# Kernel optimization log

Measured on AMD Instinct MI355X. Metric: run time of the kernel, lower is better.

## Reference

```python
import jax, jax.numpy as jnp
import numpy as np

HIDDEN = 1024
HEADS = 16
SCALE_EXP = 0.2  # module: scale = hidden_size ** (-scale)


def setup_inputs() -> dict:
    key = jax.random.key(0)
    k1, k2, k3, k4, k5 = jax.random.split(key, 5)
    b, s, h = 2, 2048, HIDDEN
    std = 1.0 / np.sqrt(h)
    return {
        "sequence_embedding": jax.random.normal(k1, (b, s, h), dtype=jnp.float32),
        "kqv_w": jax.random.normal(k2, (h, 3 * h), dtype=jnp.float32) * std,
        "kqv_b": jax.random.normal(k3, (3 * h,), dtype=jnp.float32) * std,
        "ff_w": jax.random.normal(k4, (h, h), dtype=jnp.float32) * std,
        "ff_b": jax.random.normal(k5, (h,), dtype=jnp.float32) * std,
    }


def reference(sequence_embedding, kqv_w, kqv_b, ff_w, ff_b):
    b, s, hid = sequence_embedding.shape
    d = hid // HEADS
    scale = hid ** (-SCALE_EXP)
    kqv = sequence_embedding @ kqv_w + kqv_b  # [b, s, 3h]
    k, q, v = jnp.split(kqv, 3, axis=-1)
    split_heads = lambda x: x.reshape(b, s, HEADS, d).transpose(0, 2, 1, 3)  # b h s d
    k, q, v = split_heads(k), split_heads(q), split_heads(v)
    # scores[s, n] = k_s . q_n  (rows = key pos, cols = query pos)
    scores = jnp.einsum('bhsd,bhnd->bhsn', k, q) * scale
    # faithful to source: softmax over last axis n (the QUERY axis)
    attn = jax.nn.softmax(scores, axis=-1)
    # sum over s (key positions); output indexed by n
    out = jnp.einsum('bhsn,bhsd->bhnd', attn, v)  # [b, h, s, d]
    out = out.transpose(0, 2, 1, 3).reshape(b, s, hid)
    return out @ ff_w + ff_b  # dropout is identity at inference
```

## Files before the change

kernel.cpp:

```cpp
#include <hip/hip_runtime.h>

typedef unsigned short u16;
typedef unsigned int   u32;
typedef __attribute__((ext_vector_type(8))) short s16x8;
typedef __attribute__((ext_vector_type(4))) float f32x4;

#define B_   2
#define S_   2048
#define HID  1024
#define NH   16
#define N3   3072
#define M_   4096
#define C2   0.36067376022224085f
#define OFF2 12.0f

__device__ __forceinline__ u16 f2b(float f) {
  union { float f; u32 u; } v; v.f = f;
  u32 r = (v.u + 0x7FFFu + ((v.u >> 16) & 1u)) >> 16;
  return (u16)r;
}

__device__ __forceinline__ u32 cvt_pk_bf16(float lo, float hi) {
  u32 r;
  asm("v_cvt_pk_bf16_f32 %0, %1, %2" : "=v"(r) : "v"(lo), "v"(hi));
  return r;
}

#define GLL(gp, lp)                                                          \
  __builtin_amdgcn_global_load_lds(                                          \
      (const __attribute__((address_space(1))) void*)(gp),                   \
      (__attribute__((address_space(3))) void*)(lp), 16, 0, 0)

__global__ __launch_bounds__(256) void conv_bf16(const float* __restrict__ in,
                                                 u16* __restrict__ out, int n4) {
  int i = blockIdx.x * 256 + threadIdx.x;
  if (i >= n4) return;
  float4 v = ((const float4*)in)[i];
  ushort4 o = { f2b(v.x), f2b(v.y), f2b(v.z), f2b(v.w) };
  ((ushort4*)out)[i] = o;
}

__global__ __launch_bounds__(256) void transpose_bf16(const float* __restrict__ in,
                                                      u16* __restrict__ out,
                                                      int K, int N) {
  __shared__ float T[32][33];
  const int t = threadIdx.x;
  const int k0 = blockIdx.y * 32, n0 = blockIdx.x * 32;
  {
    int r = t >> 3, c4 = (t & 7) * 4;
    float4 v = *(const float4*)(in + (size_t)(k0 + r) * N + n0 + c4);
    T[r][c4 + 0] = v.x; T[r][c4 + 1] = v.y; T[r][c4 + 2] = v.z; T[r][c4 + 3] = v.w;
  }
  __syncthreads();
  int n = t >> 3, kc = (t & 7) * 4;
  ushort4 o = { f2b(T[kc + 0][n]), f2b(T[kc + 1][n]), f2b(T[kc + 2][n]), f2b(T[kc + 3][n]) };
  *(ushort4*)(out + (size_t)(n0 + n) * K + k0 + kc) = o;
}

__global__ __launch_bounds__(256) void v_transpose(const u16* __restrict__ kqv,
                                                   u16* __restrict__ Vtg) {
  __shared__ u16 Vl[64 * 66];
  const int t = threadIdx.x;
  const int bh = blockIdx.y, b = bh >> 4, h = bh & 15;
  const int s0 = blockIdx.x * 64;
  const u16* src = kqv + (size_t)b * S_ * N3 + 2 * HID + h * 64;
  #pragma unroll
  for (int cc = 0; cc < 2; ++cc) {
    int c = t + cc * 256;
    int row = c >> 3, dc = c & 7;
    uint4 v = *(const uint4*)(src + (size_t)(s0 + row) * N3 + dc * 8);
    u32* pe = (u32*)&v;
    #pragma unroll
    for (int e = 0; e < 4; ++e)
      *(u32*)(Vl + row * 66 + dc * 8 + 2 * e) = pe[e];
  }
  __syncthreads();
  #pragma unroll
  for (int cc = 0; cc < 2; ++cc) {
    int c = t + cc * 256;
    int d = c >> 3, sc = c & 7;
    u16 tmp[8];
    #pragma unroll
    for (int j = 0; j < 8; ++j) tmp[j] = Vl[(sc * 8 + j) * 66 + d];
    *(uint4*)(Vtg + ((size_t)bh * 64 + d) * S_ + s0 + sc * 8) = *(uint4*)tmp;
  }
}

template <int OUTBF16>
__global__ __launch_bounds__(256) void gemm_bf16(const u16* __restrict__ A,
                                                 const u16* __restrict__ Bt,
                                                 const float* __restrict__ bias,
                                                 void* __restrict__ Cout,
                                                 int M, int N, int K) {
  __shared__ u16 Al[128 * 32];
  __shared__ u16 Bl[128 * 32];
  const int t = threadIdx.x, lane = t & 63, w = t >> 6;
  const int m0 = blockIdx.y * 128, n0 = blockIdx.x * 128;
  const int wm = (w >> 1) * 64, wn = (w & 1) * 64;
  const int r = lane & 15, g = lane >> 4;

  f32x4 acc[4][4];
  #pragma unroll
  for (int i = 0; i < 4; ++i)
    #pragma unroll
    for (int j = 0; j < 4; ++j) acc[i][j] = (f32x4){0.f, 0.f, 0.f, 0.f};

  const int c0 = (w << 7) + lane, c1 = c0 + 64;
  const int ar0 = c0 >> 2, ak0 = (c0 & 3) << 3;
  const int ar1 = c1 >> 2, ak1 = (c1 & 3) << 3;

  for (int k0 = 0; k0 < K; k0 += 32) {
    __syncthreads();
    GLL(A  + (size_t)(m0 + ar0) * K + k0 + ak0, Al + (w << 10));
    GLL(A  + (size_t)(m0 + ar1) * K + k0 + ak1, Al + (w << 10) + 512);
    GLL(Bt + (size_t)(n0 + ar0) * K + k0 + ak0, Bl + (w << 10));
    GLL(Bt + (size_t)(n0 + ar1) * K + k0 + ak1, Bl + (w << 10) + 512);
    __syncthreads();

    s16x8 af[4], bf[4];
    #pragma unroll
    for (int mf = 0; mf < 4; ++mf)
      af[mf] = *(const s16x8*)(Al + (wm + mf * 16 + r) * 32 + g * 8);
    #pragma unroll
    for (int nf = 0; nf < 4; ++nf)
      bf[nf] = *(const s16x8*)(Bl + (wn + nf * 16 + r) * 32 + g * 8);
    #pragma unroll
    for (int mf = 0; mf < 4; ++mf)
      #pragma unroll
      for (int nf = 0; nf < 4; ++nf)
        acc[mf][nf] = __builtin_amdgcn_mfma_f32_16x16x32_bf16(af[mf], bf[nf], acc[mf][nf], 0, 0, 0);
  }

  float bv[4];
  #pragma unroll
  for (int nf = 0; nf < 4; ++nf) bv[nf] = bias[n0 + wn + nf * 16 + r];

  #pragma unroll
  for (int mf = 0; mf < 4; ++mf)
    #pragma unroll
    for (int nf = 0; nf < 4; ++nf)
      #pragma unroll
      for (int q = 0; q < 4; ++q) {
        float o = acc[mf][nf][q] + bv[nf];
        size_t idx = (size_t)(m0 + wm + mf * 16 + 4 * g + q) * N + (n0 + wn + nf * 16 + r);
        if (OUTBF16) ((u16*)Cout)[idx] = f2b(o);
        else         ((float*)Cout)[idx] = o;
      }
}

__global__ __launch_bounds__(256) void attn_stats(const u16* __restrict__ kqv,
                                                  float* __restrict__ L2) {
  __shared__ u16 Kl[64 * 72];
  __shared__ u16 Ql[64 * 72];
  const int t = threadIdx.x, lane = t & 63, w = t >> 6;
  const int bh = blockIdx.y, b = bh >> 4, h = bh & 15;
  const int s0 = blockIdx.x * 64;
  const u16* base = kqv + (size_t)b * S_ * N3;
  const int r = lane & 15, g = lane >> 4;

  {
    int c = t;       int row = c >> 3, dc = c & 7;
    *(uint4*)(Kl + row * 72 + dc * 8) =
        *(const uint4*)(base + (size_t)(s0 + row) * N3 + h * 64 + dc * 8);
    c = t + 256;     row = c >> 3; dc = c & 7;
    *(uint4*)(Kl + row * 72 + dc * 8) =
        *(const uint4*)(base + (size_t)(s0 + row) * N3 + h * 64 + dc * 8);
  }

  float z[4] = {0.f, 0.f, 0.f, 0.f};

  for (int nt = 0; nt < 32; ++nt) {
    const int n0 = nt * 64;
    __syncthreads();
    {
      int c = t;       int row = c >> 3, dc = c & 7;
      *(uint4*)(Ql + row * 72 + dc * 8) =
          *(const uint4*)(base + (size_t)(n0 + row) * N3 + HID + h * 64 + dc * 8);
      c = t + 256;     row = c >> 3; dc = c & 7;
      *(uint4*)(Ql + row * 72 + dc * 8) =
          *(const uint4*)(base + (size_t)(n0 + row) * N3 + HID + h * 64 + dc * 8);
    }
    __syncthreads();

    s16x8 ka0 = *(const s16x8*)(Kl + (w * 16 + r) * 72 + g * 8);
    s16x8 ka1 = *(const s16x8*)(Kl + (w * 16 + r) * 72 + 32 + g * 8);
    #pragma unroll
    for (int nf = 0; nf < 4; ++nf) {
      f32x4 sc = (f32x4){0.f, 0.f, 0.f, 0.f};
      s16x8 qb0 = *(const s16x8*)(Ql + (nf * 16 + r) * 72 + g * 8);
      s16x8 qb1 = *(const s16x8*)(Ql + (nf * 16 + r) * 72 + 32 + g * 8);
      sc = __builtin_amdgcn_mfma_f32_16x16x32_bf16(ka0, qb0, sc, 0, 0, 0);
      sc = __builtin_amdgcn_mfma_f32_16x16x32_bf16(ka1, qb1, sc, 0, 0, 0);
      #pragma unroll
      for (int q = 0; q < 4; ++q)
        z[q] += exp2f(fmaf(sc[q], C2, -OFF2));
    }
  }
  #pragma unroll
  for (int m = 1; m <= 8; m <<= 1)
    #pragma unroll
    for (int q = 0; q < 4; ++q) z[q] += __shfl_xor(z[q], m);
  if (r == 0)
    #pragma unroll
    for (int q = 0; q < 4; ++q)
      L2[(size_t)bh * S_ + s0 + w * 16 + 4 * g + q] = OFF2 + log2f(z[q]);
}

__global__ __launch_bounds__(256) void attn_pv(const u16* __restrict__ kqv,
                                               const u16* __restrict__ Vtg,
                                               const float* __restrict__ L2,
                                               u16* __restrict__ attn) {
  __shared__ u16 Ql[64 * 72];
  __shared__ u16 Kl[64 * 72];
  __shared__ u16 Vl[64 * 72];
  __shared__ u16 Pl[64 * 72];
  const int t = threadIdx.x, lane = t & 63, w = t >> 6;
  const int bh = blockIdx.y, b = bh >> 4, h = bh & 15;
  const int n0 = blockIdx.x * 64;
  const u16* base = kqv + (size_t)b * S_ * N3;
  const u16* vtb  = Vtg + (size_t)bh * 64 * S_;
  const float* Lb = L2 + (size_t)bh * S_;
  const int r = lane & 15, g = lane >> 4;

  {
    int c = t;       int row = c >> 3, dc = c & 7;
    *(uint4*)(Ql + row * 72 + dc * 8) =
        *(const uint4*)(base + (size_t)(n0 + row) * N3 + HID + h * 64 + dc * 8);
    c = t + 256;     row = c >> 3; dc = c & 7;
    *(uint4*)(Ql + row * 72 + dc * 8) =
        *(const uint4*)(base + (size_t)(n0 + row) * N3 + HID + h * 64 + dc * 8);
  }
  __syncthreads();
  const s16x8 qa0 = *(const s16x8*)(Ql + (w * 16 + r) * 72 + g * 8);
  const s16x8 qa1 = *(const s16x8*)(Ql + (w * 16 + r) * 72 + 32 + g * 8);

  f32x4 oacc[4];
  #pragma unroll
  for (int i = 0; i < 4; ++i) oacc[i] = (f32x4){0.f, 0.f, 0.f, 0.f};

  for (int st = 0; st < 32; ++st) {
    const int s0 = st * 64;
    float Lv[4];
    #pragma unroll
    for (int sf = 0; sf < 4; ++sf) Lv[sf] = Lb[s0 + sf * 16 + r];

    __syncthreads();
    {
      int c = t;       int row = c >> 3, dc = c & 7;
      *(uint4*)(Kl + row * 72 + dc * 8) =
          *(const uint4*)(base + (size_t)(s0 + row) * N3 + h * 64 + dc * 8);
      c = t + 256;     row = c >> 3; dc = c & 7;
      *(uint4*)(Kl + row * 72 + dc * 8) =
          *(const uint4*)(base + (size_t)(s0 + row) * N3 + h * 64 + dc * 8);
    }
    {
      int c = t;       int row = c >> 3, dc = c & 7;
      *(uint4*)(Vl + row * 72 + dc * 8) =
          *(const uint4*)(vtb + (size_t)row * S_ + s0 + dc * 8);
      c = t + 256;     row = c >> 3; dc = c & 7;
      *(uint4*)(Vl + row * 72 + dc * 8) =
          *(const uint4*)(vtb + (size_t)row * S_ + s0 + dc * 8);
    }
    __syncthreads();

    #pragma unroll
    for (int sf = 0; sf < 4; ++sf) {
      f32x4 sc = (f32x4){0.f, 0.f, 0.f, 0.f};
      s16x8 kb0 = *(const s16x8*)(Kl + (sf * 16 + r) * 72 + g * 8);
      s16x8 kb1 = *(const s16x8*)(Kl + (sf * 16 + r) * 72 + 32 + g * 8);
      sc = __builtin_amdgcn_mfma_f32_16x16x32_bf16(qa0, kb0, sc, 0, 0, 0);
      sc = __builtin_amdgcn_mfma_f32_16x16x32_bf16(qa1, kb1, sc, 0, 0, 0);
      float p0 = exp2f(fmaf(sc[0], C2, -Lv[sf]));
      float p1 = exp2f(fmaf(sc[1], C2, -Lv[sf]));
      float p2 = exp2f(fmaf(sc[2], C2, -Lv[sf]));
      float p3 = exp2f(fmaf(sc[3], C2, -Lv[sf]));
      u32 pk01 = cvt_pk_bf16(p0, p1);
      u32 pk23 = cvt_pk_bf16(p2, p3);
      int pbase = (w * 16 + 4 * g) * 72 + sf * 16 + r;
      Pl[pbase]           = (u16)pk01;
      Pl[pbase + 72]      = (u16)(pk01 >> 16);
      Pl[pbase + 144]     = (u16)pk23;
      Pl[pbase + 216]     = (u16)(pk23 >> 16);
    }
    #pragma unroll
    for (int ks = 0; ks < 2; ++ks) {
      s16x8 pa = *(const s16x8*)(Pl + (w * 16 + r) * 72 + ks * 32 + g * 8);
      #pragma unroll
      for (int df = 0; df < 4; ++df) {
        s16x8 vb = *(const s16x8*)(Vl + (df * 16 + r) * 72 + ks * 32 + g * 8);
        oacc[df] = __builtin_amdgcn_mfma_f32_16x16x32_bf16(pa, vb, oacc[df], 0, 0, 0);
      }
    }
  }

  #pragma unroll
  for (int df = 0; df < 4; ++df)
    #pragma unroll
    for (int q = 0; q < 4; ++q)
      attn[(size_t)(b * S_ + n0 + w * 16 + 4 * g + q) * HID + h * 64 + df * 16 + r] =
          f2b(oacc[df][q]);
}

extern "C" void kernel_launch(void* const* d_in, const int* in_sizes, int n_in,
                              void* d_out, int out_size, void* d_ws, size_t ws_size,
                              hipStream_t stream) {
  const float* x     = (const float*)d_in[0];
  const float* kqv_w = (const float*)d_in[1];
  const float* kqv_b = (const float*)d_in[2];
  const float* ff_w  = (const float*)d_in[3];
  const float* ff_b  = (const float*)d_in[4];
  float* out = (float*)d_out;

  u16* xb    = (u16*)d_ws;
  u16* w1t   = xb   + (size_t)M_ * HID;
  u16* w2t   = w1t  + (size_t)N3 * HID;
  u16* kqvb  = w2t  + (size_t)HID * HID;
  u16* vtg   = kqvb + (size_t)M_ * N3;
  float* Lr  = (float*)(vtg + (size_t)B_ * NH * 64 * S_);
  u16* attnb = (u16*)(Lr + (size_t)B_ * NH * S_);

  dim3 blk(256);
  conv_bf16<<<dim3((M_ * HID / 4 + 255) / 256), blk, 0, stream>>>(x, xb, M_ * HID / 4);
  transpose_bf16<<<dim3(N3 / 32, HID / 32), blk, 0, stream>>>(kqv_w, w1t, HID, N3);
  transpose_bf16<<<dim3(HID / 32, HID / 32), blk, 0, stream>>>(ff_w, w2t, HID, HID);

  gemm_bf16<1><<<dim3(N3 / 128, M_ / 128), blk, 0, stream>>>(
      xb, w1t, kqv_b, kqvb, M_, N3, HID);

  v_transpose<<<dim3(S_ / 64, B_ * NH), blk, 0, stream>>>(kqvb, vtg);
  attn_stats <<<dim3(S_ / 64, B_ * NH), blk, 0, stream>>>(kqvb, Lr);
  attn_pv    <<<dim3(S_ / 64, B_ * NH), blk, 0, stream>>>(kqvb, vtg, Lr, attnb);

  gemm_bf16<0><<<dim3(HID / 128, M_ / 128), blk, 0, stream>>>(
      attnb, w2t, ff_b, out, M_, HID, HID);
}
```

Measured before the change: 208.6 us.

## Double per-block row tile in attention kernels, reuse Q LDS for swizzled P

Both attention kernels now process 128 rows per block instead of 64, with each wave handling two 16-row fragments. This halves the number of times each K/Q/V tile is streamed from global memory into LDS. In attn_pv the Q staging buffer is reused for P after Q is loaded into registers, and P writes and reads use an XOR swizzle to cut LDS bank conflicts. Launch bounds request 4 blocks per SM. The grid shrinks to 512 blocks, which may reduce occupancy and latency hiding, and register pressure rises from the doubled accumulators.

```diff
diff --git a/kernel.cpp b/kernel.cpp
--- a/kernel.cpp
+++ b/kernel.cpp
@@ -148,95 +148,110 @@
       }
 }
 
-__global__ __launch_bounds__(256) void attn_stats(const u16* __restrict__ kqv,
-                                                  float* __restrict__ L2) {
-  __shared__ u16 Kl[64 * 72];
+__global__ __launch_bounds__(256, 4) void attn_stats(const u16* __restrict__ kqv,
+                                                     float* __restrict__ L2) {
+  __shared__ u16 Kl[128 * 72];
   __shared__ u16 Ql[64 * 72];
   const int t = threadIdx.x, lane = t & 63, w = t >> 6;
   const int bh = blockIdx.y, b = bh >> 4, h = bh & 15;
-  const int s0 = blockIdx.x * 64;
+  const int s0 = blockIdx.x * 128;
   const u16* base = kqv + (size_t)b * S_ * N3;
   const int r = lane & 15, g = lane >> 4;
 
-  {
-    int c = t;       int row = c >> 3, dc = c & 7;
+  #pragma unroll
+  for (int cc = 0; cc < 4; ++cc) {
+    int c = t + cc * 256;
+    int row = c >> 3, dc = c & 7;
     *(uint4*)(Kl + row * 72 + dc * 8) =
         *(const uint4*)(base + (size_t)(s0 + row) * N3 + h * 64 + dc * 8);
-    c = t + 256;     row = c >> 3; dc = c & 7;
-    *(uint4*)(Kl + row * 72 + dc * 8) =
-        *(const uint4*)(base + (size_t)(s0 + row) * N3 + h * 64 + dc * 8);
-  }
-
-  float z[4] = {0.f, 0.f, 0.f, 0.f};
+  }
+  __syncthreads();
+  s16x8 ka[2][2];
+  #pragma unroll
+  for (int sf2 = 0; sf2 < 2; ++sf2) {
+    ka[sf2][0] = *(const s16x8*)(Kl + (w * 32 + sf2 * 16 + r) * 72 + g * 8);
+    ka[sf2][1] = *(const s16x8*)(Kl + (w * 32 + sf2 * 16 + r) * 72 + 32 + g * 8);
+  }
+
+  float z[2][4] = {};
 
   for (int nt = 0; nt < 32; ++nt) {
     const int n0 = nt * 64;
     __syncthreads();
-    {
-      int c = t;       int row = c >> 3, dc = c & 7;
-      *(uint4*)(Ql + row * 72 + dc * 8) =
-          *(const uint4*)(base + (size_t)(n0 + row) * N3 + HID + h * 64 + dc * 8);
-      c = t + 256;     row = c >> 3; dc = c & 7;
+    #pragma unroll
+    for (int cc = 0; cc < 2; ++cc) {
+      int c = t + cc * 256;
+      int row = c >> 3, dc = c & 7;
       *(uint4*)(Ql + row * 72 + dc * 8) =
           *(const uint4*)(base + (size_t)(n0 + row) * N3 + HID + h * 64 + dc * 8);
     }
     __syncthreads();
 
-    s16x8 ka0 = *(const s16x8*)(Kl + (w * 16 + r) * 72 + g * 8);
-    s16x8 ka1 = *(const s16x8*)(Kl + (w * 16 + r) * 72 + 32 + g * 8);
     #pragma unroll
     for (int nf = 0; nf < 4; ++nf) {
-      f32x4 sc = (f32x4){0.f, 0.f, 0.f, 0.f};
       s16x8 qb0 = *(const s16x8*)(Ql + (nf * 16 + r) * 72 + g * 8);
       s16x8 qb1 = *(const s16x8*)(Ql + (nf * 16 + r) * 72 + 32 + g * 8);
-      sc = __builtin_amdgcn_mfma_f32_16x16x32_bf16(ka0, qb0, sc, 0, 0, 0);
-      sc = __builtin_amdgcn_mfma_f32_16x16x32_bf16(ka1, qb1, sc, 0, 0, 0);
+      #pragma unroll
+      for (int sf2 = 0; sf2 < 2; ++sf2) {
+        f32x4 sc = (f32x4){0.f, 0.f, 0.f, 0.f};
+        sc = __builtin_amdgcn_mfma_f32_16x16x32_bf16(ka[sf2][0], qb0, sc, 0, 0, 0);
+        sc = __builtin_amdgcn_mfma_f32_16x16x32_bf16(ka[sf2][1], qb1, sc, 0, 0, 0);
+        #pragma unroll
+        for (int q = 0; q < 4; ++q)
+          z[sf2][q] += exp2f(fmaf(sc[q], C2, -OFF2));
+      }
+    }
+  }
+  #pragma unroll
+  for (int m = 1; m <= 8; m <<= 1)
+    #pragma unroll
+    for (int sf2 = 0; sf2 < 2; ++sf2)
+      #pragma unroll
+      for (int q = 0; q < 4; ++q) z[sf2][q] += __shfl_xor(z[sf2][q], m);
+  if (r == 0)
+    #pragma unroll
+    for (int sf2 = 0; sf2 < 2; ++sf2)
       #pragma unroll
       for (int q = 0; q < 4; ++q)
-        z[q] += exp2f(fmaf(sc[q], C2, -OFF2));
-    }
-  }
-  #pragma unroll
-  for (int m = 1; m <= 8; m <<= 1)
-    #pragma unroll
-    for (int q = 0; q < 4; ++q) z[q] += __shfl_xor(z[q], m);
-  if (r == 0)
-    #pragma unroll
-    for (int q = 0; q < 4; ++q)
-      L2[(size_t)bh * S_ + s0 + w * 16 + 4 * g + q] = OFF2 + log2f(z[q]);
-}
-
-__global__ __launch_bounds__(256) void attn_pv(const u16* __restrict__ kqv,
-                                               const u16* __restrict__ Vtg,
-                                               const float* __restrict__ L2,
-                                               u16* __restrict__ attn) {
-  __shared__ u16 Ql[64 * 72];
+        L2[(size_t)bh * S_ + s0 + w * 32 + sf2 * 16 + 4 * g + q] =
+            OFF2 + log2f(z[sf2][q]);
+}
+
+__global__ __launch_bounds__(256, 4) void attn_pv(const u16* __restrict__ kqv,
+                                                  const u16* __restrict__ Vtg,
+                                                  const float* __restrict__ L2,
+                                                  u16* __restrict__ attn) {
+  __shared__ u16 QPl[128 * 72];
   __shared__ u16 Kl[64 * 72];
   __shared__ u16 Vl[64 * 72];
-  __shared__ u16 Pl[64 * 72];
   const int t = threadIdx.x, lane = t & 63, w = t >> 6;
   const int bh = blockIdx.y, b = bh >> 4, h = bh & 15;
-  const int n0 = blockIdx.x * 64;
+  const int n0 = blockIdx.x * 128;
   const u16* base = kqv + (size_t)b * S_ * N3;
   const u16* vtb  = Vtg + (size_t)bh * 64 * S_;
   const float* Lb = L2 + (size_t)bh * S_;
   const int r = lane & 15, g = lane >> 4;
 
-  {
-    int c = t;       int row = c >> 3, dc = c & 7;
-    *(uint4*)(Ql + row * 72 + dc * 8) =
+  #pragma unroll
+  for (int cc = 0; cc < 4; ++cc) {
+    int c = t + cc * 256;
+    int row = c >> 3, dc = c & 7;
+    *(uint4*)(QPl + row * 72 + dc * 8) =
         *(const uint4*)(base + (size_t)(n0 + row) * N3 + HID + h * 64 + dc * 8);
-    c = t + 256;     row = c >> 3; dc = c & 7;
-    *(uint4*)(Ql + row * 72 + dc * 8) =
-        *(const uint4*)(base + (size_t)(n0 + row) * N3 + HID + h * 64 + dc * 8);
   }
   __syncthreads();
-  const s16x8 qa0 = *(const s16x8*)(Ql + (w * 16 + r) * 72 + g * 8);
-  const s16x8 qa1 = *(const s16x8*)(Ql + (w * 16 + r) * 72 + 32 + g * 8);
-
-  f32x4 oacc[4];
-  #pragma unroll
-  for (int i = 0; i < 4; ++i) oacc[i] = (f32x4){0.f, 0.f, 0.f, 0.f};
+  s16x8 qa[2][2];
+  #pragma unroll
+  for (int nf2 = 0; nf2 < 2; ++nf2) {
+    qa[nf2][0] = *(const s16x8*)(QPl + (w * 32 + nf2 * 16 + r) * 72 + g * 8);
+    qa[nf2][1] = *(const s16x8*)(QPl + (w * 32 + nf2 * 16 + r) * 72 + 32 + g * 8);
+  }
+
+  f32x4 oacc[2][4];
+  #pragma unroll
+  for (int i = 0; i < 2; ++i)
+    #pragma unroll
+    for (int j = 0; j < 4; ++j) oacc[i][j] = (f32x4){0.f, 0.f, 0.f, 0.f};
 
   for (int st = 0; st < 32; ++st) {
     const int s0 = st * 64;
@@ -245,60 +260,61 @@
     for (int sf = 0; sf < 4; ++sf) Lv[sf] = Lb[s0 + sf * 16 + r];
 
     __syncthreads();
-    {
-      int c = t;       int row = c >> 3, dc = c & 7;
+    #pragma unroll
+    for (int cc = 0; cc < 2; ++cc) {
+      int c = t + cc * 256;
+      int row = c >> 3, dc = c & 7;
       *(uint4*)(Kl + row * 72 + dc * 8) =
           *(const uint4*)(base + (size_t)(s0 + row) * N3 + h * 64 + dc * 8);
-      c = t + 256;     row = c >> 3; dc = c & 7;
-      *(uint4*)(Kl + row * 72 + dc * 8) =
-          *(const uint4*)(base + (size_t)(s0 + row) * N3 + h * 64 + dc * 8);
-    }
-    {
-      int c = t;       int row = c >> 3, dc = c & 7;
-      *(uint4*)(Vl + row * 72 + dc * 8) =
-          *(const uint4*)(vtb + (size_t)row * S_ + s0 + dc * 8);
-      c = t + 256;     row = c >> 3; dc = c & 7;
       *(uint4*)(Vl + row * 72 + dc * 8) =
           *(const uint4*)(vtb + (size_t)row * S_ + s0 + dc * 8);
     }
     __syncthreads();
 
     #pragma unroll
-    for (int sf = 0; sf < 4; ++sf) {
-      f32x4 sc = (f32x4){0.f, 0.f, 0.f, 0.f};
-      s16x8 kb0 = *(const s16x8*)(Kl + (sf * 16 + r) * 72 + g * 8);
-      s16x8 kb1 = *(const s16x8*)(Kl + (sf * 16 + r) * 72 + 32 + g * 8);
-      sc = __builtin_amdgcn_mfma_f32_16x16x32_bf16(qa0, kb0, sc, 0, 0, 0);
-      sc = __builtin_amdgcn_mfma_f32_16x16x32_bf16(qa1, kb1, sc, 0, 0, 0);
-      float p0 = exp2f(fmaf(sc[0], C2, -Lv[sf]));
-      float p1 = exp2f(fmaf(sc[1], C2, -Lv[sf]));
-      float p2 = exp2f(fmaf(sc[2], C2, -Lv[sf]));
-      float p3 = exp2f(fmaf(sc[3], C2, -Lv[sf]));
-      u32 pk01 = cvt_pk_bf16(p0, p1);
-      u32 pk23 = cvt_pk_bf16(p2, p3);
-      int pbase = (w * 16 + 4 * g) * 72 + sf * 16 + r;
-      Pl[pbase]           = (u16)pk01;
-      Pl[pbase + 72]      = (u16)(pk01 >> 16);
-      Pl[pbase + 144]     = (u16)pk23;
-      Pl[pbase + 216]     = (u16)(pk23 >> 16);
-    }
-    #pragma unroll
-    for (int ks = 0; ks < 2; ++ks) {
-      s16x8 pa = *(const s16x8*)(Pl + (w * 16 + r) * 72 + ks * 32 + g * 8);
-      #pragma unroll
-      for (int df = 0; df < 4; ++df) {
-        s16x8 vb = *(const s16x8*)(Vl + (df * 16 + r) * 72 + ks * 32 + g * 8);
-        oacc[df] = __builtin_amdgcn_mfma_f32_16x16x32_bf16(pa, vb, oacc[df], 0, 0, 0);
+    for (int nf2 = 0; nf2 < 2; ++nf2)
+      #pragma unroll
+      for (int sf = 0; sf < 4; ++sf) {
+        f32x4 sc = (f32x4){0.f, 0.f, 0.f, 0.f};
+        s16x8 kb0 = *(const s16x8*)(Kl + (sf * 16 + r) * 72 + g * 8);
+        s16x8 kb1 = *(const s16x8*)(Kl + (sf * 16 + r) * 72 + 32 + g * 8);
+        sc = __builtin_amdgcn_mfma_f32_16x16x32_bf16(qa[nf2][0], kb0, sc, 0, 0, 0);
+        sc = __builtin_amdgcn_mfma_f32_16x16x32_bf16(qa[nf2][1], kb1, sc, 0, 0, 0);
+        float p0 = exp2f(fmaf(sc[0], C2, -Lv[sf]));
+        float p1 = exp2f(fmaf(sc[1], C2, -Lv[sf]));
+        float p2 = exp2f(fmaf(sc[2], C2, -Lv[sf]));
+        float p3 = exp2f(fmaf(sc[3], C2, -Lv[sf]));
+        u32 pk01 = cvt_pk_bf16(p0, p1);
+        u32 pk23 = cvt_pk_bf16(p2, p3);
+        int pc = (sf * 2 + (r >> 3)) ^ (2 * g);
+        int pbase = (w * 32 + nf2 * 16 + 4 * g) * 72 + pc * 8 + (r & 7);
+        QPl[pbase]       = (u16)pk01;
+        QPl[pbase + 72]  = (u16)(pk01 >> 16);
+        QPl[pbase + 144] = (u16)pk23;
+        QPl[pbase + 216] = (u16)(pk23 >> 16);
       }
-    }
-  }
-
-  #pragma unroll
-  for (int df = 0; df < 4; ++df)
-    #pragma unroll
-    for (int q = 0; q < 4; ++q)
-      attn[(size_t)(b * S_ + n0 + w * 16 + 4 * g + q) * HID + h * 64 + df * 16 + r] =
-          f2b(oacc[df][q]);
+    #pragma unroll
+    for (int nf2 = 0; nf2 < 2; ++nf2)
+      #pragma unroll
+      for (int ks = 0; ks < 2; ++ks) {
+        s16x8 pa = *(const s16x8*)(QPl + (w * 32 + nf2 * 16 + r) * 72 +
+                                   ((ks * 4 + g) ^ (2 * (r >> 2))) * 8);
+        #pragma unroll
+        for (int df = 0; df < 4; ++df) {
+          s16x8 vb = *(const s16x8*)(Vl + (df * 16 + r) * 72 + ks * 32 + g * 8);
+          oacc[nf2][df] = __builtin_amdgcn_mfma_f32_16x16x32_bf16(pa, vb, oacc[nf2][df], 0, 0, 0);
+        }
+      }
+  }
+
+  #pragma unroll
+  for (int nf2 = 0; nf2 < 2; ++nf2)
+    #pragma unroll
+    for (int df = 0; df < 4; ++df)
+      #pragma unroll
+      for (int q = 0; q < 4; ++q)
+        attn[(size_t)(b * S_ + n0 + w * 32 + nf2 * 16 + 4 * g + q) * HID +
+             h * 64 + df * 16 + r] = f2b(oacc[nf2][df][q]);
 }
 
 extern "C" void kernel_launch(void* const* d_in, const int* in_sizes, int n_in,
@@ -328,8 +344,8 @@
       xb, w1t, kqv_b, kqvb, M_, N3, HID);
 
   v_transpose<<<dim3(S_ / 64, B_ * NH), blk, 0, stream>>>(kqvb, vtg);
-  attn_stats <<<dim3(S_ / 64, B_ * NH), blk, 0, stream>>>(kqvb, Lr);
-  attn_pv    <<<dim3(S_ / 64, B_ * NH), blk, 0, stream>>>(kqvb, vtg, Lr, attnb);
+  attn_stats <<<dim3(S_ / 128, B_ * NH), blk, 0, stream>>>(kqvb, Lr);
+  attn_pv    <<<dim3(S_ / 128, B_ * NH), blk, 0, stream>>>(kqvb, vtg, Lr, attnb);
 
   gemm_bf16<0><<<dim3(HID / 128, M_ / 128), blk, 0, stream>>>(
       attnb, w2t, ff_b, out, M_, HID, HID);
```

New measurement: 206.1 us. No clear change (-1.2%).

## Double-buffer K/V/Q tiles in attention kernels with register prefetch

Applied to the files above, without the earlier changes.

Both attention kernels now prefetch the next tile's Q (stats) or K and V (pv) into registers before computing on the current LDS buffer, then write the prefetched data into a second LDS buffer and use one barrier per iteration instead of two. This hides global load latency behind the MFMA and exp work. The pv kernel also reuses the Q staging buffer for P and applies an XOR swizzle to P's layout to reduce LDS bank conflicts. It costs more LDS per block and more registers held across the loop, which may reduce occupancy.

```diff
diff --git a/kernel.cpp b/kernel.cpp
--- a/kernel.cpp
+++ b/kernel.cpp
@@ -151,50 +151,53 @@
 __global__ __launch_bounds__(256) void attn_stats(const u16* __restrict__ kqv,
                                                   float* __restrict__ L2) {
   __shared__ u16 Kl[64 * 72];
-  __shared__ u16 Ql[64 * 72];
+  __shared__ u16 Ql[2][64 * 72];
   const int t = threadIdx.x, lane = t & 63, w = t >> 6;
   const int bh = blockIdx.y, b = bh >> 4, h = bh & 15;
   const int s0 = blockIdx.x * 64;
   const u16* base = kqv + (size_t)b * S_ * N3;
   const int r = lane & 15, g = lane >> 4;
-
-  {
-    int c = t;       int row = c >> 3, dc = c & 7;
-    *(uint4*)(Kl + row * 72 + dc * 8) =
-        *(const uint4*)(base + (size_t)(s0 + row) * N3 + h * 64 + dc * 8);
-    c = t + 256;     row = c >> 3; dc = c & 7;
-    *(uint4*)(Kl + row * 72 + dc * 8) =
-        *(const uint4*)(base + (size_t)(s0 + row) * N3 + h * 64 + dc * 8);
-  }
+  const int srow = t >> 3, sdc = t & 7;
+
+  *(uint4*)(Kl + srow * 72 + sdc * 8) =
+      *(const uint4*)(base + (size_t)(s0 + srow) * N3 + h * 64 + sdc * 8);
+  *(uint4*)(Kl + (srow + 32) * 72 + sdc * 8) =
+      *(const uint4*)(base + (size_t)(s0 + srow + 32) * N3 + h * 64 + sdc * 8);
+  *(uint4*)(Ql[0] + srow * 72 + sdc * 8) =
+      *(const uint4*)(base + (size_t)srow * N3 + HID + h * 64 + sdc * 8);
+  *(uint4*)(Ql[0] + (srow + 32) * 72 + sdc * 8) =
+      *(const uint4*)(base + (size_t)(srow + 32) * N3 + HID + h * 64 + sdc * 8);
+  __syncthreads();
+
+  const s16x8 ka0 = *(const s16x8*)(Kl + (w * 16 + r) * 72 + g * 8);
+  const s16x8 ka1 = *(const s16x8*)(Kl + (w * 16 + r) * 72 + 32 + g * 8);
 
   float z[4] = {0.f, 0.f, 0.f, 0.f};
 
   for (int nt = 0; nt < 32; ++nt) {
-    const int n0 = nt * 64;
-    __syncthreads();
-    {
-      int c = t;       int row = c >> 3, dc = c & 7;
-      *(uint4*)(Ql + row * 72 + dc * 8) =
-          *(const uint4*)(base + (size_t)(n0 + row) * N3 + HID + h * 64 + dc * 8);
-      c = t + 256;     row = c >> 3; dc = c & 7;
-      *(uint4*)(Ql + row * 72 + dc * 8) =
-          *(const uint4*)(base + (size_t)(n0 + row) * N3 + HID + h * 64 + dc * 8);
-    }
-    __syncthreads();
-
-    s16x8 ka0 = *(const s16x8*)(Kl + (w * 16 + r) * 72 + g * 8);
-    s16x8 ka1 = *(const s16x8*)(Kl + (w * 16 + r) * 72 + 32 + g * 8);
+    const int cur = nt & 1;
+    uint4 qr0, qr1;
+    if (nt < 31) {
+      const int n1 = (nt + 1) * 64;
+      qr0 = *(const uint4*)(base + (size_t)(n1 + srow) * N3 + HID + h * 64 + sdc * 8);
+      qr1 = *(const uint4*)(base + (size_t)(n1 + srow + 32) * N3 + HID + h * 64 + sdc * 8);
+    }
     #pragma unroll
     for (int nf = 0; nf < 4; ++nf) {
+      s16x8 qb0 = *(const s16x8*)(Ql[cur] + (nf * 16 + r) * 72 + g * 8);
+      s16x8 qb1 = *(const s16x8*)(Ql[cur] + (nf * 16 + r) * 72 + 32 + g * 8);
       f32x4 sc = (f32x4){0.f, 0.f, 0.f, 0.f};
-      s16x8 qb0 = *(const s16x8*)(Ql + (nf * 16 + r) * 72 + g * 8);
-      s16x8 qb1 = *(const s16x8*)(Ql + (nf * 16 + r) * 72 + 32 + g * 8);
       sc = __builtin_amdgcn_mfma_f32_16x16x32_bf16(ka0, qb0, sc, 0, 0, 0);
       sc = __builtin_amdgcn_mfma_f32_16x16x32_bf16(ka1, qb1, sc, 0, 0, 0);
       #pragma unroll
       for (int q = 0; q < 4; ++q)
         z[q] += exp2f(fmaf(sc[q], C2, -OFF2));
     }
+    if (nt < 31) {
+      *(uint4*)(Ql[cur ^ 1] + srow * 72 + sdc * 8) = qr0;
+      *(uint4*)(Ql[cur ^ 1] + (srow + 32) * 72 + sdc * 8) = qr1;
+    }
+    __syncthreads();
   }
   #pragma unroll
   for (int m = 1; m <= 8; m <<= 1)
@@ -210,10 +213,9 @@
                                                const u16* __restrict__ Vtg,
                                                const float* __restrict__ L2,
                                                u16* __restrict__ attn) {
-  __shared__ u16 Ql[64 * 72];
-  __shared__ u16 Kl[64 * 72];
-  __shared__ u16 Vl[64 * 72];
-  __shared__ u16 Pl[64 * 72];
+  __shared__ u16 QPl[64 * 72];
+  __shared__ u16 Kl[2][64 * 72];
+  __shared__ u16 Vl[2][64 * 72];
   const int t = threadIdx.x, lane = t & 63, w = t >> 6;
   const int bh = blockIdx.y, b = bh >> 4, h = bh & 15;
   const int n0 = blockIdx.x * 64;
@@ -221,53 +223,49 @@
   const u16* vtb  = Vtg + (size_t)bh * 64 * S_;
   const float* Lb = L2 + (size_t)bh * S_;
   const int r = lane & 15, g = lane >> 4;
-
-  {
-    int c = t;       int row = c >> 3, dc = c & 7;
-    *(uint4*)(Ql + row * 72 + dc * 8) =
-        *(const uint4*)(base + (size_t)(n0 + row) * N3 + HID + h * 64 + dc * 8);
-    c = t + 256;     row = c >> 3; dc = c & 7;
-    *(uint4*)(Ql + row * 72 + dc * 8) =
-        *(const uint4*)(base + (size_t)(n0 + row) * N3 + HID + h * 64 + dc * 8);
-  }
+  const int srow = t >> 3, sdc = t & 7;
+
+  *(uint4*)(QPl + srow * 72 + sdc * 8) =
+      *(const uint4*)(base + (size_t)(n0 + srow) * N3 + HID + h * 64 + sdc * 8);
+  *(uint4*)(QPl + (srow + 32) * 72 + sdc * 8) =
+      *(const uint4*)(base + (size_t)(n0 + srow + 32) * N3 + HID + h * 64 + sdc * 8);
+  *(uint4*)(Kl[0] + srow * 72 + sdc * 8) =
+      *(const uint4*)(base + (size_t)srow * N3 + h * 64 + sdc * 8);
+  *(uint4*)(Kl[0] + (srow + 32) * 72 + sdc * 8) =
+      *(const uint4*)(base + (size_t)(srow + 32) * N3 + h * 64 + sdc * 8);
+  *(uint4*)(Vl[0] + srow * 72 + sdc * 8) =
+      *(const uint4*)(vtb + (size_t)srow * S_ + sdc * 8);
+  *(uint4*)(Vl[0] + (srow + 32) * 72 + sdc * 8) =
+      *(const uint4*)(vtb + (size_t)(srow + 32) * S_ + sdc * 8);
   __syncthreads();
-  const s16x8 qa0 = *(const s16x8*)(Ql + (w * 16 + r) * 72 + g * 8);
-  const s16x8 qa1 = *(const s16x8*)(Ql + (w * 16 + r) * 72 + 32 + g * 8);
+
+  const s16x8 qa0 = *(const s16x8*)(QPl + (w * 16 + r) * 72 + g * 8);
+  const s16x8 qa1 = *(const s16x8*)(QPl + (w * 16 + r) * 72 + 32 + g * 8);
 
   f32x4 oacc[4];
   #pragma unroll
   for (int i = 0; i < 4; ++i) oacc[i] = (f32x4){0.f, 0.f, 0.f, 0.f};
 
   for (int st = 0; st < 32; ++st) {
+    const int cur = st & 1;
     const int s0 = st * 64;
+    uint4 kr0, kr1, vr0, vr1;
+    if (st < 31) {
+      const int s1 = s0 + 64;
+      kr0 = *(const uint4*)(base + (size_t)(s1 + srow) * N3 + h * 64 + sdc * 8);
+      kr1 = *(const uint4*)(base + (size_t)(s1 + srow + 32) * N3 + h * 64 + sdc * 8);
+      vr0 = *(const uint4*)(vtb + (size_t)srow * S_ + s1 + sdc * 8);
+      vr1 = *(const uint4*)(vtb + (size_t)(srow + 32) * S_ + s1 + sdc * 8);
+    }
     float Lv[4];
     #pragma unroll
     for (int sf = 0; sf < 4; ++sf) Lv[sf] = Lb[s0 + sf * 16 + r];
-
-    __syncthreads();
-    {
-      int c = t;       int row = c >> 3, dc = c & 7;
-      *(uint4*)(Kl + row * 72 + dc * 8) =
-          *(const uint4*)(base + (size_t)(s0 + row) * N3 + h * 64 + dc * 8);
-      c = t + 256;     row = c >> 3; dc = c & 7;
-      *(uint4*)(Kl + row * 72 + dc * 8) =
-          *(const uint4*)(base + (size_t)(s0 + row) * N3 + h * 64 + dc * 8);
-    }
-    {
-      int c = t;       int row = c >> 3, dc = c & 7;
-      *(uint4*)(Vl + row * 72 + dc * 8) =
-          *(const uint4*)(vtb + (size_t)row * S_ + s0 + dc * 8);
-      c = t + 256;     row = c >> 3; dc = c & 7;
-      *(uint4*)(Vl + row * 72 + dc * 8) =
-          *(const uint4*)(vtb + (size_t)row * S_ + s0 + dc * 8);
-    }
-    __syncthreads();
 
     #pragma unroll
     for (int sf = 0; sf < 4; ++sf) {
       f32x4 sc = (f32x4){0.f, 0.f, 0.f, 0.f};
-      s16x8 kb0 = *(const s16x8*)(Kl + (sf * 16 + r) * 72 + g * 8);
-      s16x8 kb1 = *(const s16x8*)(Kl + (sf * 16 + r) * 72 + 32 + g * 8);
+      s16x8 kb0 = *(const s16x8*)(Kl[cur] + (sf * 16 + r) * 72 + g * 8);
+      s16x8 kb1 = *(const s16x8*)(Kl[cur] + (sf * 16 + r) * 72 + 32 + g * 8);
       sc = __builtin_amdgcn_mfma_f32_16x16x32_bf16(qa0, kb0, sc, 0, 0, 0);
       sc = __builtin_amdgcn_mfma_f32_16x16x32_bf16(qa1, kb1, sc, 0, 0, 0);
       float p0 = exp2f(fmaf(sc[0], C2, -Lv[sf]));
@@ -276,21 +274,30 @@
       float p3 = exp2f(fmaf(sc[3], C2, -Lv[sf]));
       u32 pk01 = cvt_pk_bf16(p0, p1);
       u32 pk23 = cvt_pk_bf16(p2, p3);
-      int pbase = (w * 16 + 4 * g) * 72 + sf * 16 + r;
-      Pl[pbase]           = (u16)pk01;
-      Pl[pbase + 72]      = (u16)(pk01 >> 16);
-      Pl[pbase + 144]     = (u16)pk23;
-      Pl[pbase + 216]     = (u16)(pk23 >> 16);
+      int pc = (sf * 2 + (r >> 3)) ^ (2 * g);
+      int pbase = (w * 16 + 4 * g) * 72 + pc * 8 + (r & 7);
+      QPl[pbase]       = (u16)pk01;
+      QPl[pbase + 72]  = (u16)(pk01 >> 16);
+      QPl[pbase + 144] = (u16)pk23;
+      QPl[pbase + 216] = (u16)(pk23 >> 16);
     }
     #pragma unroll
     for (int ks = 0; ks < 2; ++ks) {
-      s16x8 pa = *(const s16x8*)(Pl + (w * 16 + r) * 72 + ks * 32 + g * 8);
+      s16x8 pa = *(const s16x8*)(QPl + (w * 16 + r) * 72 +
+                                 ((ks * 4 + g) ^ (2 * (r >> 2))) * 8);
       #pragma unroll
       for (int df = 0; df < 4; ++df) {
-        s16x8 vb = *(const s16x8*)(Vl + (df * 16 + r) * 72 + ks * 32 + g * 8);
+        s16x8 vb = *(const s16x8*)(Vl[cur] + (df * 16 + r) * 72 + ks * 32 + g * 8);
         oacc[df] = __builtin_amdgcn_mfma_f32_16x16x32_bf16(pa, vb, oacc[df], 0, 0, 0);
       }
     }
+    if (st < 31) {
+      *(uint4*)(Kl[cur ^ 1] + srow * 72 + sdc * 8) = kr0;
+      *(uint4*)(Kl[cur ^ 1] + (srow + 32) * 72 + sdc * 8) = kr1;
+      *(uint4*)(Vl[cur ^ 1] + srow * 72 + sdc * 8) = vr0;
+      *(uint4*)(Vl[cur ^ 1] + (srow + 32) * 72 + sdc * 8) = vr1;
+    }
+    __syncthreads();
   }
 
   #pragma unroll
```

Measured after the change: 212.8 us. +2.0%, slower.

## Split attention across key halves, fold normalizer into V, swizzle P tile

Applied to the files above, without the earlier changes.

The softmax normalizer is moved out of the PV loop. Stats kernels accumulate row sums into a zeroed buffer with atomics, and V is pre-divided by them during its transpose. Both the stats and PV kernels now split the sequence across two z-blocks to double grid parallelism, and a combine kernel adds the two bf16 partial outputs. PV also reuses the Q LDS buffer for P with an XOR swizzle and adds MFMA priority hints. The cost is an extra bf16 rounding of the partials, extra launches, and an atomic reduction.

```diff
diff --git a/kernel.cpp b/kernel.cpp
--- a/kernel.cpp
+++ b/kernel.cpp
@@ -18,6 +18,11 @@
   union { float f; u32 u; } v; v.f = f;
   u32 r = (v.u + 0x7FFFu + ((v.u >> 16) & 1u)) >> 16;
   return (u16)r;
+}
+
+__device__ __forceinline__ float b2f(u16 x) {
+  union { u32 u; float f; } v; v.u = (u32)x << 16;
+  return v.f;
 }
 
 __device__ __forceinline__ u32 cvt_pk_bf16(float lo, float hi) {
@@ -57,8 +62,13 @@
   *(ushort4*)(out + (size_t)(n0 + n) * K + k0 + kc) = o;
 }
 
-__global__ __launch_bounds__(256) void v_transpose(const u16* __restrict__ kqv,
-                                                   u16* __restrict__ Vtg) {
+__global__ __launch_bounds__(256) void zero_f32(float* __restrict__ p) {
+  ((float4*)p)[blockIdx.x * 256 + threadIdx.x] = (float4){0.f, 0.f, 0.f, 0.f};
+}
+
+__global__ __launch_bounds__(256) void v_transpose_scaled(const u16* __restrict__ kqv,
+                                                          const float* __restrict__ zacc,
+                                                          u16* __restrict__ Vtg) {
   __shared__ u16 Vl[64 * 66];
   const int t = threadIdx.x;
   const int bh = blockIdx.y, b = bh >> 4, h = bh & 15;
@@ -79,9 +89,13 @@
   for (int cc = 0; cc < 2; ++cc) {
     int c = t + cc * 256;
     int d = c >> 3, sc = c & 7;
+    float4 za = *(const float4*)(zacc + (size_t)bh * S_ + s0 + sc * 8);
+    float4 zb = *(const float4*)(zacc + (size_t)bh * S_ + s0 + sc * 8 + 4);
+    float zi[8] = { za.x, za.y, za.z, za.w, zb.x, zb.y, zb.z, zb.w };
     u16 tmp[8];
     #pragma unroll
-    for (int j = 0; j < 8; ++j) tmp[j] = Vl[(sc * 8 + j) * 66 + d];
+    for (int j = 0; j < 8; ++j)
+      tmp[j] = f2b(b2f(Vl[(sc * 8 + j) * 66 + d]) / zi[j]);
     *(uint4*)(Vtg + ((size_t)bh * 64 + d) * S_ + s0 + sc * 8) = *(uint4*)tmp;
   }
 }
@@ -149,12 +163,13 @@
 }
 
 __global__ __launch_bounds__(256) void attn_stats(const u16* __restrict__ kqv,
-                                                  float* __restrict__ L2) {
+                                                  float* __restrict__ zacc) {
   __shared__ u16 Kl[64 * 72];
   __shared__ u16 Ql[64 * 72];
   const int t = threadIdx.x, lane = t & 63, w = t >> 6;
   const int bh = blockIdx.y, b = bh >> 4, h = bh & 15;
   const int s0 = blockIdx.x * 64;
+  const int nbase = blockIdx.z * (S_ / 2);
   const u16* base = kqv + (size_t)b * S_ * N3;
   const int r = lane & 15, g = lane >> 4;
 
@@ -166,11 +181,14 @@
     *(uint4*)(Kl + row * 72 + dc * 8) =
         *(const uint4*)(base + (size_t)(s0 + row) * N3 + h * 64 + dc * 8);
   }
+  __syncthreads();
+  const s16x8 ka0 = *(const s16x8*)(Kl + (w * 16 + r) * 72 + g * 8);
+  const s16x8 ka1 = *(const s16x8*)(Kl + (w * 16 + r) * 72 + 32 + g * 8);
 
   float z[4] = {0.f, 0.f, 0.f, 0.f};
 
-  for (int nt = 0; nt < 32; ++nt) {
-    const int n0 = nt * 64;
+  for (int nt = 0; nt < 16; ++nt) {
+    const int n0 = nbase + nt * 64;
     __syncthreads();
     {
       int c = t;       int row = c >> 3, dc = c & 7;
@@ -182,15 +200,15 @@
     }
     __syncthreads();
 
-    s16x8 ka0 = *(const s16x8*)(Kl + (w * 16 + r) * 72 + g * 8);
-    s16x8 ka1 = *(const s16x8*)(Kl + (w * 16 + r) * 72 + 32 + g * 8);
     #pragma unroll
     for (int nf = 0; nf < 4; ++nf) {
-      f32x4 sc = (f32x4){0.f, 0.f, 0.f, 0.f};
       s16x8 qb0 = *(const s16x8*)(Ql + (nf * 16 + r) * 72 + g * 8);
       s16x8 qb1 = *(const s16x8*)(Ql + (nf * 16 + r) * 72 + 32 + g * 8);
+      f32x4 sc = (f32x4){0.f, 0.f, 0.f, 0.f};
+      __builtin_amdgcn_s_setprio(1);
       sc = __builtin_amdgcn_mfma_f32_16x16x32_bf16(ka0, qb0, sc, 0, 0, 0);
       sc = __builtin_amdgcn_mfma_f32_16x16x32_bf16(ka1, qb1, sc, 0, 0, 0);
+      __builtin_amdgcn_s_setprio(0);
       #pragma unroll
       for (int q = 0; q < 4; ++q)
         z[q] += exp2f(fmaf(sc[q], C2, -OFF2));
@@ -203,61 +221,52 @@
   if (r == 0)
     #pragma unroll
     for (int q = 0; q < 4; ++q)
-      L2[(size_t)bh * S_ + s0 + w * 16 + 4 * g + q] = OFF2 + log2f(z[q]);
+      atomicAdd(zacc + (size_t)bh * S_ + s0 + w * 16 + 4 * g + q, z[q]);
 }
 
 __global__ __launch_bounds__(256) void attn_pv(const u16* __restrict__ kqv,
                                                const u16* __restrict__ Vtg,
-                                               const float* __restrict__ L2,
-                                               u16* __restrict__ attn) {
-  __shared__ u16 Ql[64 * 72];
+                                               u16* __restrict__ p0,
+                                               u16* __restrict__ p1) {
+  __shared__ u16 QPl[64 * 72];
   __shared__ u16 Kl[64 * 72];
   __shared__ u16 Vl[64 * 72];
-  __shared__ u16 Pl[64 * 72];
   const int t = threadIdx.x, lane = t & 63, w = t >> 6;
   const int bh = blockIdx.y, b = bh >> 4, h = bh & 15;
   const int n0 = blockIdx.x * 64;
+  const int sbase = blockIdx.z * 16;
   const u16* base = kqv + (size_t)b * S_ * N3;
   const u16* vtb  = Vtg + (size_t)bh * 64 * S_;
-  const float* Lb = L2 + (size_t)bh * S_;
   const int r = lane & 15, g = lane >> 4;
 
   {
     int c = t;       int row = c >> 3, dc = c & 7;
-    *(uint4*)(Ql + row * 72 + dc * 8) =
+    *(uint4*)(QPl + row * 72 + dc * 8) =
         *(const uint4*)(base + (size_t)(n0 + row) * N3 + HID + h * 64 + dc * 8);
     c = t + 256;     row = c >> 3; dc = c & 7;
-    *(uint4*)(Ql + row * 72 + dc * 8) =
+    *(uint4*)(QPl + row * 72 + dc * 8) =
         *(const uint4*)(base + (size_t)(n0 + row) * N3 + HID + h * 64 + dc * 8);
   }
   __syncthreads();
-  const s16x8 qa0 = *(const s16x8*)(Ql + (w * 16 + r) * 72 + g * 8);
-  const s16x8 qa1 = *(const s16x8*)(Ql + (w * 16 + r) * 72 + 32 + g * 8);
+  const s16x8 qa0 = *(const s16x8*)(QPl + (w * 16 + r) * 72 + g * 8);
+  const s16x8 qa1 = *(const s16x8*)(QPl + (w * 16 + r) * 72 + 32 + g * 8);
 
   f32x4 oacc[4];
   #pragma unroll
   for (int i = 0; i < 4; ++i) oacc[i] = (f32x4){0.f, 0.f, 0.f, 0.f};
 
-  for (int st = 0; st < 32; ++st) {
-    const int s0 = st * 64;
-    float Lv[4];
-    #pragma unroll
-    for (int sf = 0; sf < 4; ++sf) Lv[sf] = Lb[s0 + sf * 16 + r];
-
+  for (int st = 0; st < 16; ++st) {
+    const int s0 = (sbase + st) * 64;
     __syncthreads();
     {
       int c = t;       int row = c >> 3, dc = c & 7;
       *(uint4*)(Kl + row * 72 + dc * 8) =
           *(const uint4*)(base + (size_t)(s0 + row) * N3 + h * 64 + dc * 8);
+      *(uint4*)(Vl + row * 72 + dc * 8) =
+          *(const uint4*)(vtb + (size_t)row * S_ + s0 + dc * 8);
       c = t + 256;     row = c >> 3; dc = c & 7;
       *(uint4*)(Kl + row * 72 + dc * 8) =
           *(const uint4*)(base + (size_t)(s0 + row) * N3 + h * 64 + dc * 8);
-    }
-    {
-      int c = t;       int row = c >> 3, dc = c & 7;
-      *(uint4*)(Vl + row * 72 + dc * 8) =
-          *(const uint4*)(vtb + (size_t)row * S_ + s0 + dc * 8);
-      c = t + 256;     row = c >> 3; dc = c & 7;
       *(uint4*)(Vl + row * 72 + dc * 8) =
           *(const uint4*)(vtb + (size_t)row * S_ + s0 + dc * 8);
     }
@@ -268,37 +277,57 @@
       f32x4 sc = (f32x4){0.f, 0.f, 0.f, 0.f};
       s16x8 kb0 = *(const s16x8*)(Kl + (sf * 16 + r) * 72 + g * 8);
       s16x8 kb1 = *(const s16x8*)(Kl + (sf * 16 + r) * 72 + 32 + g * 8);
+      __builtin_amdgcn_s_setprio(1);
       sc = __builtin_amdgcn_mfma_f32_16x16x32_bf16(qa0, kb0, sc, 0, 0, 0);
       sc = __builtin_amdgcn_mfma_f32_16x16x32_bf16(qa1, kb1, sc, 0, 0, 0);
-      float p0 = exp2f(fmaf(sc[0], C2, -Lv[sf]));
-      float p1 = exp2f(fmaf(sc[1], C2, -Lv[sf]));
-      float p2 = exp2f(fmaf(sc[2], C2, -Lv[sf]));
-      float p3 = exp2f(fmaf(sc[3], C2, -Lv[sf]));
-      u32 pk01 = cvt_pk_bf16(p0, p1);
-      u32 pk23 = cvt_pk_bf16(p2, p3);
-      int pbase = (w * 16 + 4 * g) * 72 + sf * 16 + r;
-      Pl[pbase]           = (u16)pk01;
-      Pl[pbase + 72]      = (u16)(pk01 >> 16);
-      Pl[pbase + 144]     = (u16)pk23;
-      Pl[pbase + 216]     = (u16)(pk23 >> 16);
-    }
+      __builtin_amdgcn_s_setprio(0);
+      float pp0 = exp2f(fmaf(sc[0], C2, -OFF2));
+      float pp1 = exp2f(fmaf(sc[1], C2, -OFF2));
+      float pp2 = exp2f(fmaf(sc[2], C2, -OFF2));
+      float pp3 = exp2f(fmaf(sc[3], C2, -OFF2));
+      u32 pk01 = cvt_pk_bf16(pp0, pp1);
+      u32 pk23 = cvt_pk_bf16(pp2, pp3);
+      int pc = (sf * 2 + (r >> 3)) ^ (2 * g);
+      int pbase = (w * 16 + 4 * g) * 72 + pc * 8 + (r & 7);
+      QPl[pbase]       = (u16)pk01;
+      QPl[pbase + 72]  = (u16)(pk01 >> 16);
+      QPl[pbase + 144] = (u16)pk23;
+      QPl[pbase + 216] = (u16)(pk23 >> 16);
+    }
+    __builtin_amdgcn_s_setprio(1);
     #pragma unroll
     for (int ks = 0; ks < 2; ++ks) {
-      s16x8 pa = *(const s16x8*)(Pl + (w * 16 + r) * 72 + ks * 32 + g * 8);
+      s16x8 pa = *(const s16x8*)(QPl + (w * 16 + r) * 72 +
+                                 ((ks * 4 + g) ^ (2 * (r >> 2))) * 8);
       #pragma unroll
       for (int df = 0; df < 4; ++df) {
         s16x8 vb = *(const s16x8*)(Vl + (df * 16 + r) * 72 + ks * 32 + g * 8);
         oacc[df] = __builtin_amdgcn_mfma_f32_16x16x32_bf16(pa, vb, oacc[df], 0, 0, 0);
       }
     }
-  }
-
+    __builtin_amdgcn_s_setprio(0);
+  }
+
+  u16* dst = blockIdx.z ? p1 : p0;
   #pragma unroll
   for (int df = 0; df < 4; ++df)
     #pragma unroll
     for (int q = 0; q < 4; ++q)
-      attn[(size_t)(b * S_ + n0 + w * 16 + 4 * g + q) * HID + h * 64 + df * 16 + r] =
+      dst[(size_t)(b * S_ + n0 + w * 16 + 4 * g + q) * HID + h * 64 + df * 16 + r] =
           f2b(oacc[df][q]);
+}
+
+__global__ __launch_bounds__(256) void combine_halves(u16* __restrict__ p0,
+                                                      const u16* __restrict__ p1) {
+  int i = blockIdx.x * 256 + threadIdx.x;
+  uint4 a = ((const uint4*)p0)[i];
+  uint4 bq = ((const uint4*)p1)[i];
+  const u16* ae = (const u16*)&a;
+  const u16* be = (const u16*)&bq;
+  u16 o[8];
+  #pragma unroll
+  for (int j = 0; j < 8; ++j) o[j] = f2b(b2f(ae[j]) + b2f(be[j]));
+  ((uint4*)p0)[i] = *(uint4*)o;
 }
 
 extern "C" void kernel_launch(void* const* d_in, const int* in_sizes, int n_in,
@@ -316,20 +345,22 @@
   u16* w2t   = w1t  + (size_t)N3 * HID;
   u16* kqvb  = w2t  + (size_t)HID * HID;
   u16* vtg   = kqvb + (size_t)M_ * N3;
-  float* Lr  = (float*)(vtg + (size_t)B_ * NH * 64 * S_);
-  u16* attnb = (u16*)(Lr + (size_t)B_ * NH * S_);
+  float* zac = (float*)(vtg + (size_t)B_ * NH * 64 * S_);
+  u16* attnb = (u16*)(zac + (size_t)B_ * NH * S_);
 
   dim3 blk(256);
-  conv_bf16<<<dim3((M_ * HID / 4 + 255) / 256), blk, 0, stream>>>(x, xb, M_ * HID / 4);
+  conv_bf16<<<dim3(M_ * HID / 4 / 256), blk, 0, stream>>>(x, xb, M_ * HID / 4);
   transpose_bf16<<<dim3(N3 / 32, HID / 32), blk, 0, stream>>>(kqv_w, w1t, HID, N3);
   transpose_bf16<<<dim3(HID / 32, HID / 32), blk, 0, stream>>>(ff_w, w2t, HID, HID);
 
   gemm_bf16<1><<<dim3(N3 / 128, M_ / 128), blk, 0, stream>>>(
       xb, w1t, kqv_b, kqvb, M_, N3, HID);
 
-  v_transpose<<<dim3(S_ / 64, B_ * NH), blk, 0, stream>>>(kqvb, vtg);
-  attn_stats <<<dim3(S_ / 64, B_ * NH), blk, 0, stream>>>(kqvb, Lr);
-  attn_pv    <<<dim3(S_ / 64, B_ * NH), blk, 0, stream>>>(kqvb, vtg, Lr, attnb);
+  zero_f32<<<dim3(B_ * NH * S_ / 4 / 256), blk, 0, stream>>>(zac);
+  attn_stats<<<dim3(S_ / 64, B_ * NH, 2), blk, 0, stream>>>(kqvb, zac);
+  v_transpose_scaled<<<dim3(S_ / 64, B_ * NH), blk, 0, stream>>>(kqvb, zac, vtg);
+  attn_pv<<<dim3(S_ / 64, B_ * NH, 2), blk, 0, stream>>>(kqvb, vtg, attnb, xb);
+  combine_halves<<<dim3(M_ * HID / 8 / 256), blk, 0, stream>>>(attnb, xb);
 
   gemm_bf16<0><<<dim3(HID / 128, M_ / 128), blk, 0, stream>>>(
       attnb, w2t, ff_b, out, M_, HID, HID);
```

Measured after the change: 201.8 us. -3.2%, faster.
